# Optimization experiments

Measured on AMD Instinct MI355X. Metric: run time of the kernel, lower is better.

## Reference

```python
import jax, jax.numpy as jnp
import numpy as np

B, TQ, TV, H = 8, 2048, 2048, 1024
LN_EPS = 1e-5


def setup_inputs() -> dict:
    key = jax.random.key(0)
    k1, k2, k3, k4 = jax.random.split(key, 4)
    query = jax.random.normal(k1, (B, TQ, H), dtype=jnp.float32)
    value = jax.random.normal(k2, (B, TV, H), dtype=jnp.float32)
    # nn.Linear(2H -> H): weight [H, 2H], bias [H]
    bound = 1.0 / np.sqrt(2 * H)
    W = jax.random.uniform(k3, (H, 2 * H), minval=-bound, maxval=bound, dtype=jnp.float32)
    b = jax.random.uniform(k4, (H,), minval=-bound, maxval=bound, dtype=jnp.float32)
    gamma = jnp.ones((H,), dtype=jnp.float32)
    beta = jnp.zeros((H,), dtype=jnp.float32)
    return {"query": query, "value": value, "W": W, "b": b, "gamma": gamma, "beta": beta}


def reference(query, value, W, b, gamma, beta):
    # scores: [B, Tq, Tv]
    score = jnp.einsum("bqh,bvh->bqv", query, value)
    attn = jax.nn.softmax(score, axis=-1)
    context = jnp.einsum("bqv,bvh->bqh", attn, value)  # [B, Tq, H]
    combined = jnp.concatenate((context, query), axis=2)  # [B, Tq, 2H]
    proj = jnp.einsum("bqk,hk->bqh", combined, W) + b  # [B, Tq, H]
    mean = jnp.mean(proj, axis=-1, keepdims=True)
    var = jnp.mean(jnp.square(proj - mean), axis=-1, keepdims=True)
    out = (proj - mean) * jax.lax.rsqrt(var + LN_EPS) * gamma + beta
    return out
```

## Files before the change

### kernel.cpp

```cpp
#include <hip/hip_runtime.h>

typedef unsigned short u16;
typedef _Float16 f16;
typedef __attribute__((ext_vector_type(8))) _Float16 f16x8;
typedef __attribute__((ext_vector_type(4))) float f32x4;

#define B_  8
#define TQ_ 2048
#define TV_ 2048
#define H_  1024

__device__ __forceinline__ u16 f2h(float x) {
    union { f16 h; u16 u; } c; c.h = (f16)x; return c.u;
}

__device__ __forceinline__ void gload_lds16(const u16* g, u16* l) {
    typedef __attribute__((address_space(1))) const unsigned short GAS;
    typedef __attribute__((address_space(3))) unsigned short LAS;
    __builtin_amdgcn_global_load_lds((GAS*)g, (LAS*)l, 16, 0, 0);
}

__global__ __launch_bounds__(256) void k_cvt(const float4* __restrict__ x,
                                             ushort4* __restrict__ o) {
    long long i = (long long)blockIdx.x * 256 + threadIdx.x;
    float4 v = x[i];
    ushort4 h;
    h.x = f2h(v.x); h.y = f2h(v.y); h.z = f2h(v.z); h.w = f2h(v.w);
    o[i] = h;
}

__global__ __launch_bounds__(256) void k_cvt_q(const float4* __restrict__ q4,
                                               u16* __restrict__ CQ) {
    long long i = (long long)blockIdx.x * 256 + threadIdx.x;
    float4 x = q4[i];
    ushort4 h;
    h.x = f2h(x.x); h.y = f2h(x.y); h.z = f2h(x.z); h.w = f2h(x.w);
    long long row = i >> 8;
    int col = (int)(i & 255) * 4;
    *(ushort4*)(CQ + row * 2048 + 1024 + col) = h;
}

__global__ __launch_bounds__(256) void k_cvt_vt(const float* __restrict__ v,
                                                u16* __restrict__ Vh,
                                                u16* __restrict__ VT) {
    __shared__ u16 s[64][65];
    const int t = threadIdx.x;
    const int c0 = blockIdx.x * 64;
    const int r0 = blockIdx.y * 64;
    const long long zb = (long long)blockIdx.z * (2048LL * 1024LL);
    const float* ib = v + zb;
#pragma unroll
    for (int it = 0; it < 4; ++it) {
        int rl = it * 16 + (t >> 4);
        int cl = (t & 15) * 4;
        float4 x = *(const float4*)(ib + (long long)(r0 + rl) * 1024 + c0 + cl);
        ushort4 h;
        h.x = f2h(x.x); h.y = f2h(x.y); h.z = f2h(x.z); h.w = f2h(x.w);
        *(ushort4*)(Vh + zb + (long long)(r0 + rl) * 1024 + c0 + cl) = h;
        s[rl][cl + 0] = h.x; s[rl][cl + 1] = h.y; s[rl][cl + 2] = h.z; s[rl][cl + 3] = h.w;
    }
    __syncthreads();
#pragma unroll
    for (int it = 0; it < 4; ++it) {
        int cl = it * 16 + (t >> 4);
        int rl = (t & 15) * 4;
        ushort4 o;
        o.x = s[rl + 0][cl]; o.y = s[rl + 1][cl]; o.z = s[rl + 2][cl]; o.w = s[rl + 3][cl];
        *(ushort4*)(VT + zb + (long long)(c0 + cl) * 2048 + r0 + rl) = o;
    }
}

struct GemmPass {
    const u16* A; const u16* B;
    long long sA; long long sB;
    int lda; int ldb;
};

template<int NH, int OM>
__global__ __launch_bounds__(512, 2) void k_gemm8(GemmPass p0,
                                                  int K, int mnTiles, int gn,
                                                  void* __restrict__ Cv, long long sC,
                                                  int ldc, const float* __restrict__ bias) {
    constexpr int BUFU = 16384 + NH * 8192;
    __shared__ __align__(16) u16 lds[2 * BUFU];

    const int nper = gridDim.x >> 3;
    const int g = (blockIdx.x & 7) * nper + (blockIdx.x >> 3);
    const int z = g / mnTiles;
    const int rem = g - z * mnTiles;
    const int bm = (rem / gn) * 256;
    const int bn = (rem % gn) * (NH * 128);

    const int tid = threadIdx.x;
    const int lane = tid & 63, wid = tid >> 6;
    const int wm = wid >> 2, wn = wid & 3;
    const int l16 = lane & 15, kg = lane >> 4;

    f32x4 acc[8][NH * 2];
    f32x4 zv = {0.f, 0.f, 0.f, 0.f};
#pragma unroll
    for (int i = 0; i < 8; ++i)
#pragma unroll
        for (int j = 0; j < NH * 2; ++j) acc[i][j] = zv;

    const u16* Ab = p0.A + (long long)z * p0.sA;
    const u16* Bb = p0.B + (long long)z * p0.sB;
    const int lda = p0.lda, ldb = p0.ldb;
    const int NT = K >> 6;

    auto stage = [&](const u16* Xb, int ld, int R0, int k0, int h, int rbase) {
#pragma unroll
        for (int c = 0; c < 2; ++c) {
            int i = c * 512 + tid;
            int rl = i >> 3, js = i & 7;
            int r = h * 128 + rl;
            int j = js ^ (r & 7);
            gload_lds16(Xb + (long long)(R0 + r) * ld + k0 + j * 8,
                        &lds[rbase + h * 8192 + i * 8]);
        }
    };
    auto rdA = [&](int base, int mh, f16x8* dst) {
#pragma unroll
        for (int i = 0; i < 4; ++i) {
            int r = wm * 128 + mh * 64 + i * 16 + l16;
#pragma unroll
            for (int ks = 0; ks < 2; ++ks) {
                int js = (ks * 4 + kg) ^ (r & 7);
                dst[i * 2 + ks] = *(const f16x8*)&lds[base + r * 64 + js * 8];
            }
        }
    };
    auto rdB = [&](int base, int nh, f16x8* dst) {
#pragma unroll
        for (int jn = 0; jn < 2; ++jn) {
            int r = wn * (NH * 32) + nh * 32 + jn * 16 + l16;
#pragma unroll
            for (int ks = 0; ks < 2; ++ks) {
                int js = (ks * 4 + kg) ^ (r & 7);
                dst[jn * 2 + ks] = *(const f16x8*)&lds[base + r * 64 + js * 8];
            }
        }
    };

    stage(Ab, lda, bm, 0, 0, 0);
    stage(Ab, lda, bm, 0, 1, 0);
#pragma unroll
    for (int h = 0; h < NH; ++h) stage(Bb, ldb, bn, 0, h, 16384);
    if (NT > 1) {
#pragma unroll
        for (int h = 0; h < NH; ++h) stage(Bb, ldb, bn, 64, h, BUFU + 16384);
        if constexpr (NH == 2) asm volatile("s_waitcnt vmcnt(4)" ::: "memory");
        else                   asm volatile("s_waitcnt vmcnt(2)" ::: "memory");
    } else {
        asm volatile("s_waitcnt vmcnt(0)" ::: "memory");
    }
    __builtin_amdgcn_s_barrier();

    f16x8 a0[8], a1[8], b0[4], b1[4];
    for (int t = 0; t < NT; ++t) {
        const int cur = t & 1;
        const int Abase = cur * BUFU;
        const int Bbase = Abase + 16384;
        const int OA = (cur ^ 1) * BUFU;
        const bool sa = (t + 1) < NT;
        const bool sb = (t + 2) < NT;
        if constexpr (NH == 2) {
            rdA(Abase, 0, a0);
            rdB(Bbase, 0, b0);
            if (sa) stage(Ab, lda, bm, (t + 1) * 64, 0, OA);
            __builtin_amdgcn_s_barrier();
            __builtin_amdgcn_s_setprio(1);
#pragma unroll
            for (int i = 0; i < 4; ++i)
#pragma unroll
                for (int jn = 0; jn < 2; ++jn)
#pragma unroll
                    for (int ks = 0; ks < 2; ++ks)
                        acc[i][jn] = __builtin_amdgcn_mfma_f32_16x16x32_f16(a0[i * 2 + ks], b0[jn * 2 + ks], acc[i][jn], 0, 0, 0);
            __builtin_amdgcn_s_setprio(0);
            __builtin_amdgcn_s_barrier();
            rdB(Bbase, 1, b1);
            if (sa) stage(Ab, lda, bm, (t + 1) * 64, 1, OA);
            __builtin_amdgcn_s_barrier();
            __builtin_amdgcn_s_setprio(1);
#pragma unroll
            for (int i = 0; i < 4; ++i)
#pragma unroll
                for (int jn = 0; jn < 2; ++jn)
#pragma unroll
                    for (int ks = 0; ks < 2; ++ks)
                        acc[i][2 + jn] = __builtin_amdgcn_mfma_f32_16x16x32_f16(a0[i * 2 + ks], b1[jn * 2 + ks], acc[i][2 + jn], 0, 0, 0);
            __builtin_amdgcn_s_setprio(0);
            __builtin_amdgcn_s_barrier();
            rdA(Abase, 1, a1);
            if (sb) stage(Bb, ldb, bn, (t + 2) * 64, 0, Bbase);
            __builtin_amdgcn_s_barrier();
            __builtin_amdgcn_s_setprio(1);
#pragma unroll
            for (int i = 0; i < 4; ++i)
#pragma unroll
                for (int jn = 0; jn < 2; ++jn)
#pragma unroll
                    for (int ks = 0; ks < 2; ++ks)
                        acc[4 + i][2 + jn] = __builtin_amdgcn_mfma_f32_16x16x32_f16(a1[i * 2 + ks], b1[jn * 2 + ks], acc[4 + i][2 + jn], 0, 0, 0);
            __builtin_amdgcn_s_setprio(0);
            __builtin_amdgcn_s_barrier();
            if (sb) {
                stage(Bb, ldb, bn, (t + 2) * 64, 1, Bbase);
                asm volatile("s_waitcnt vmcnt(4)" ::: "memory");
            } else if (sa) {
                asm volatile("s_waitcnt vmcnt(0)" ::: "memory");
            }
            __builtin_amdgcn_s_barrier();
            __builtin_amdgcn_s_setprio(1);
#pragma unroll
            for (int i = 0; i < 4; ++i)
#pragma unroll
                for (int jn = 0; jn < 2; ++jn)
#pragma unroll
                    for (int ks = 0; ks < 2; ++ks)
                        acc[4 + i][jn] = __builtin_amdgcn_mfma_f32_16x16x32_f16(a1[i * 2 + ks], b0[jn * 2 + ks], acc[4 + i][jn], 0, 0, 0);
            __builtin_amdgcn_s_setprio(0);
            __builtin_amdgcn_s_barrier();
        } else {
            rdA(Abase, 0, a0);
            rdB(Bbase, 0, b0);
            if (sa) stage(Ab, lda, bm, (t + 1) * 64, 0, OA);
            __builtin_amdgcn_s_barrier();
            __builtin_amdgcn_s_setprio(1);
#pragma unroll
            for (int i = 0; i < 4; ++i)
#pragma unroll
                for (int jn = 0; jn < 2; ++jn)
#pragma unroll
                    for (int ks = 0; ks < 2; ++ks)
                        acc[i][jn] = __builtin_amdgcn_mfma_f32_16x16x32_f16(a0[i * 2 + ks], b0[jn * 2 + ks], acc[i][jn], 0, 0, 0);
            __builtin_amdgcn_s_setprio(0);
            __builtin_amdgcn_s_barrier();
            rdA(Abase, 1, a1);
            if (sa) stage(Ab, lda, bm, (t + 1) * 64, 1, OA);
            if (sb) {
                stage(Bb, ldb, bn, (t + 2) * 64, 0, Bbase);
                asm volatile("s_waitcnt vmcnt(2)" ::: "memory");
            } else if (sa) {
                asm volatile("s_waitcnt vmcnt(0)" ::: "memory");
            }
            __builtin_amdgcn_s_barrier();
            __builtin_amdgcn_s_setprio(1);
#pragma unroll
            for (int i = 0; i < 4; ++i)
#pragma unroll
                for (int jn = 0; jn < 2; ++jn)
#pragma unroll
                    for (int ks = 0; ks < 2; ++ks)
                        acc[4 + i][jn] = __builtin_amdgcn_mfma_f32_16x16x32_f16(a1[i * 2 + ks], b0[jn * 2 + ks], acc[4 + i][jn], 0, 0, 0);
            __builtin_amdgcn_s_setprio(0);
            __builtin_amdgcn_s_barrier();
        }
    }

    const int colBase = bn + wn * (NH * 32);
    const int rowBase = bm + wm * 128;
#pragma unroll
    for (int mi = 0; mi < 8; ++mi) {
#pragma unroll
        for (int nj = 0; nj < NH * 2; ++nj) {
            int col = colBase + nj * 16 + l16;
            float badd = bias ? bias[col] : 0.f;
#pragma unroll
            for (int r = 0; r < 4; ++r) {
                long long row = rowBase + mi * 16 + kg * 4 + r;
                long long idx = (long long)z * sC + row * (long long)ldc + col;
                float vv = acc[mi][nj][r] + badd;
                if constexpr (OM == 1) ((u16*)Cv)[idx] = f2h(vv);
                else ((float*)Cv)[idx] = vv;
            }
        }
    }
}

__global__ __launch_bounds__(256) void k_softmax(const float* __restrict__ S,
                                                 u16* __restrict__ P, int mode) {
    int q, zc;
    if (mode == 2) {
        int x = blockIdx.x & 7;
        zc = x >> 2;
        q = ((x & 3) << 9) | (blockIdx.x >> 3);
    } else {
        zc = 0;
        q = blockIdx.x;
    }
    const float* row = S + ((long long)zc * TQ_ + q) * TV_;
    u16* prow = P + ((long long)zc * TQ_ + q) * TV_;
    int t = threadIdx.x;
    float4 a = *(const float4*)(row + t * 4);
    float4 c = *(const float4*)(row + 1024 + t * 4);
    float m = fmaxf(fmaxf(fmaxf(a.x, a.y), fmaxf(a.z, a.w)),
                    fmaxf(fmaxf(c.x, c.y), fmaxf(c.z, c.w)));
#pragma unroll
    for (int o = 32; o; o >>= 1) m = fmaxf(m, __shfl_xor(m, o));
    __shared__ float rm[4], rs[4];
    if ((t & 63) == 0) rm[t >> 6] = m;
    __syncthreads();
    m = fmaxf(fmaxf(rm[0], rm[1]), fmaxf(rm[2], rm[3]));
    float e0 = __expf(a.x - m), e1 = __expf(a.y - m), e2 = __expf(a.z - m), e3 = __expf(a.w - m);
    float e4 = __expf(c.x - m), e5 = __expf(c.y - m), e6 = __expf(c.z - m), e7 = __expf(c.w - m);
    float s = ((e0 + e1) + (e2 + e3)) + ((e4 + e5) + (e6 + e7));
#pragma unroll
    for (int o = 32; o; o >>= 1) s += __shfl_xor(s, o);
    if ((t & 63) == 0) rs[t >> 6] = s;
    __syncthreads();
    s = rs[0] + rs[1] + rs[2] + rs[3];
    float inv = 1.f / s;
    ushort4 o0, o1;
    o0.x = f2h(e0 * inv); o0.y = f2h(e1 * inv); o0.z = f2h(e2 * inv); o0.w = f2h(e3 * inv);
    o1.x = f2h(e4 * inv); o1.y = f2h(e5 * inv); o1.z = f2h(e6 * inv); o1.w = f2h(e7 * inv);
    *(ushort4*)(prow + t * 4) = o0;
    *(ushort4*)(prow + 1024 + t * 4) = o1;
}

__global__ __launch_bounds__(256) void k_layernorm(float* __restrict__ O,
                                                   const float* __restrict__ g,
                                                   const float* __restrict__ b) {
    float* row = O + (long long)blockIdx.x * H_;
    int t = threadIdx.x;
    float4 x = *(const float4*)(row + t * 4);
    float s1 = x.x + x.y + x.z + x.w;
    float s2 = x.x * x.x + x.y * x.y + x.z * x.z + x.w * x.w;
#pragma unroll
    for (int o = 32; o; o >>= 1) { s1 += __shfl_xor(s1, o); s2 += __shfl_xor(s2, o); }
    __shared__ float r1[4], r2[4];
    if ((t & 63) == 0) { r1[t >> 6] = s1; r2[t >> 6] = s2; }
    __syncthreads();
    s1 = r1[0] + r1[1] + r1[2] + r1[3];
    s2 = r2[0] + r2[1] + r2[2] + r2[3];
    float mean = s1 * (1.f / H_);
    float var = s2 * (1.f / H_) - mean * mean;
    float rstd = rsqrtf(fmaxf(var, 0.f) + 1e-5f);
    float4 gv = *(const float4*)(g + t * 4);
    float4 bv = *(const float4*)(b + t * 4);
    float4 o;
    o.x = (x.x - mean) * rstd * gv.x + bv.x;
    o.y = (x.y - mean) * rstd * gv.y + bv.y;
    o.z = (x.z - mean) * rstd * gv.z + bv.z;
    o.w = (x.w - mean) * rstd * gv.w + bv.w;
    *(float4*)(row + t * 4) = o;
}

extern "C" void kernel_launch(void* const* d_in, const int* in_sizes, int n_in,
                              void* d_out, int out_size, void* d_ws, size_t ws_size,
                              hipStream_t stream) {
    const float* q     = (const float*)d_in[0];
    const float* v     = (const float*)d_in[1];
    const float* W     = (const float*)d_in[2];
    const float* bias  = (const float*)d_in[3];
    const float* gamma = (const float*)d_in[4];
    const float* beta  = (const float*)d_in[5];
    float* out = (float*)d_out;
    char* ws = (char*)d_ws;

    const long long nQV = (long long)B_ * TQ_ * H_;
    const long long nW  = (long long)H_ * 2 * H_;
    const long long nCQ = (long long)B_ * TQ_ * 2048;
    const long long nP  = (long long)B_ * TQ_ * TV_;

    u16* Vh = (u16*)ws;
    u16* VT = Vh + nQV;
    u16* Wh = VT + nQV;
    u16* CQ = Wh + nW;
    u16* Pa = CQ + nCQ;
    float* S = (float*)(Pa + nP);
    size_t fixedBytes = (size_t)((char*)S - ws);
    const size_t perZ = (size_t)TQ_ * TV_ * 4;

    int Zc = (fixedBytes + 2 * perZ <= ws_size) ? 2 : 1;

    k_cvt_q<<<dim3(nQV / 4 / 256), dim3(256), 0, stream>>>((const float4*)q, CQ);
    k_cvt  <<<dim3(nW / 4 / 256),  dim3(256), 0, stream>>>((const float4*)W, (ushort4*)Wh);
    k_cvt_vt<<<dim3(H_ / 64, TV_ / 64, B_), dim3(256), 0, stream>>>(v, Vh, VT);

    for (int c0 = 0; c0 < B_; c0 += Zc) {
        GemmPass s0{CQ + (long long)c0 * TQ_ * 2048 + 1024,
                    Vh + (long long)c0 * TV_ * H_,
                    (long long)TQ_ * 2048, (long long)TV_ * H_, 2048, H_};
        k_gemm8<1, 0><<<dim3(Zc * 128), dim3(512), 0, stream>>>(
            s0, H_, 128, 16, S, (long long)TQ_ * TV_, TV_, nullptr);
        k_softmax<<<dim3(Zc * TQ_), dim3(256), 0, stream>>>(
            S, Pa + (long long)c0 * TQ_ * TV_, Zc);
    }

    GemmPass pv{Pa, VT, (long long)TQ_ * TV_, (long long)H_ * TV_, TV_, TV_};
    k_gemm8<2, 1><<<dim3(256), dim3(512), 0, stream>>>(
        pv, TV_, 32, 4, CQ, (long long)TQ_ * 2048, 2048, nullptr);

    GemmPass j0{CQ, Wh, 0, 0, 2048, 2 * H_};
    k_gemm8<2, 0><<<dim3(256), dim3(512), 0, stream>>>(
        j0, 2 * H_, 256, 4, out, 0, H_, bias);

    k_layernorm<<<dim3(B_ * TQ_), dim3(256), 0, stream>>>(out, gamma, beta);
}
```

Before: 352.2 us.

## Write softmax probabilities in place over scores and run PV per chunk

Softmax now writes its fp16 probabilities into the same buffer as the fp32 scores, using a row stride of 4096 halfs. A barrier before the write keeps the in-place overwrite safe. This removes the separate P buffer, which frees workspace so up to 4 batches can be chunked at a time. The PV GEMM now runs inside the chunk loop on the chunk's scores while they may still be in cache, and both A-stage halves are issued earlier in the GEMM main loop. The costs are more, smaller PV launches with different tile parameters, a strided A read, and changed load/wait ordering in the GEMM pipeline.

Result: faster. 341.7 us (-3.0%).

```diff
diff --git a/kernel.cpp b/kernel.cpp
--- a/kernel.cpp
+++ b/kernel.cpp
@@ -225,7 +225,10 @@
         } else {
             rdA(Abase, 0, a0);
             rdB(Bbase, 0, b0);
-            if (sa) stage(Ab, lda, bm, (t + 1) * 64, 0, OA);
+            if (sa) {
+                stage(Ab, lda, bm, (t + 1) * 64, 0, OA);
+                stage(Ab, lda, bm, (t + 1) * 64, 1, OA);
+            }
             __builtin_amdgcn_s_barrier();
             __builtin_amdgcn_s_setprio(1);
 #pragma unroll
@@ -238,7 +241,6 @@
             __builtin_amdgcn_s_setprio(0);
             __builtin_amdgcn_s_barrier();
             rdA(Abase, 1, a1);
-            if (sa) stage(Ab, lda, bm, (t + 1) * 64, 1, OA);
             if (sb) {
                 stage(Bb, ldb, bn, (t + 2) * 64, 0, Bbase);
                 asm volatile("s_waitcnt vmcnt(2)" ::: "memory");
@@ -279,19 +281,9 @@
     }
 }
 
-__global__ __launch_bounds__(256) void k_softmax(const float* __restrict__ S,
-                                                 u16* __restrict__ P, int mode) {
-    int q, zc;
-    if (mode == 2) {
-        int x = blockIdx.x & 7;
-        zc = x >> 2;
-        q = ((x & 3) << 9) | (blockIdx.x >> 3);
-    } else {
-        zc = 0;
-        q = blockIdx.x;
-    }
-    const float* row = S + ((long long)zc * TQ_ + q) * TV_;
-    u16* prow = P + ((long long)zc * TQ_ + q) * TV_;
+__global__ __launch_bounds__(256) void k_softmax(float* __restrict__ S) {
+    float* row = S + (long long)blockIdx.x * TV_;
+    u16* prow = (u16*)row;
     int t = threadIdx.x;
     float4 a = *(const float4*)(row + t * 4);
     float4 c = *(const float4*)(row + 1024 + t * 4);
@@ -315,6 +307,7 @@
     ushort4 o0, o1;
     o0.x = f2h(e0 * inv); o0.y = f2h(e1 * inv); o0.z = f2h(e2 * inv); o0.w = f2h(e3 * inv);
     o1.x = f2h(e4 * inv); o1.y = f2h(e5 * inv); o1.z = f2h(e6 * inv); o1.w = f2h(e7 * inv);
+    __syncthreads();
     *(ushort4*)(prow + t * 4) = o0;
     *(ushort4*)(prow + 1024 + t * 4) = o1;
 }
@@ -362,18 +355,19 @@
     const long long nQV = (long long)B_ * TQ_ * H_;
     const long long nW  = (long long)H_ * 2 * H_;
     const long long nCQ = (long long)B_ * TQ_ * 2048;
-    const long long nP  = (long long)B_ * TQ_ * TV_;
 
     u16* Vh = (u16*)ws;
     u16* VT = Vh + nQV;
     u16* Wh = VT + nQV;
     u16* CQ = Wh + nW;
-    u16* Pa = CQ + nCQ;
-    float* S = (float*)(Pa + nP);
+    float* S = (float*)(CQ + nCQ);
     size_t fixedBytes = (size_t)((char*)S - ws);
     const size_t perZ = (size_t)TQ_ * TV_ * 4;
 
-    int Zc = (fixedBytes + 2 * perZ <= ws_size) ? 2 : 1;
+    int Zc = 1;
+    for (int cand = 4; cand >= 1; cand >>= 1) {
+        if (fixedBytes + (size_t)cand * perZ <= ws_size) { Zc = cand; break; }
+    }
 
     k_cvt_q<<<dim3(nQV / 4 / 256), dim3(256), 0, stream>>>((const float4*)q, CQ);
     k_cvt  <<<dim3(nW / 4 / 256),  dim3(256), 0, stream>>>((const float4*)W, (ushort4*)Wh);
@@ -385,13 +379,12 @@
                     (long long)TQ_ * 2048, (long long)TV_ * H_, 2048, H_};
         k_gemm8<1, 0><<<dim3(Zc * 128), dim3(512), 0, stream>>>(
             s0, H_, 128, 16, S, (long long)TQ_ * TV_, TV_, nullptr);
-        k_softmax<<<dim3(Zc * TQ_), dim3(256), 0, stream>>>(
-            S, Pa + (long long)c0 * TQ_ * TV_, Zc);
-    }
-
-    GemmPass pv{Pa, VT, (long long)TQ_ * TV_, (long long)H_ * TV_, TV_, TV_};
-    k_gemm8<2, 1><<<dim3(256), dim3(512), 0, stream>>>(
-        pv, TV_, 32, 4, CQ, (long long)TQ_ * 2048, 2048, nullptr);
+        k_softmax<<<dim3(Zc * TQ_), dim3(256), 0, stream>>>(S);
+        GemmPass pv{(const u16*)S, VT + (long long)c0 * H_ * TV_,
+                    (long long)TQ_ * 4096, (long long)H_ * TV_, 4096, TV_};
+        k_gemm8<1, 1><<<dim3(Zc * 64), dim3(512), 0, stream>>>(
+            pv, TV_, 64, 8, CQ + (long long)c0 * TQ_ * 2048, (long long)TQ_ * 2048, 2048, nullptr);
+    }
 
     GemmPass j0{CQ, Wh, 0, 0, 2048, 2 * H_};
     k_gemm8<2, 0><<<dim3(256), dim3(512), 0, stream>>>(
```
